# Performance work log

Measured on AMD Instinct MI355X. Metric: run time of the kernel, lower is better.

The kernel has to match this reference:

```python
import jax, jax.numpy as jnp
import numpy as np

D_MODEL = 1024
NHEAD = 16
HEAD_DIM = D_MODEL // NHEAD
D_FF = 4096
EPS = 1e-5


def _layernorm(x, g, b):
    mu = jnp.mean(x, axis=-1, keepdims=True)
    var = jnp.mean(jnp.square(x - mu), axis=-1, keepdims=True)
    return (x - mu) * jax.lax.rsqrt(var + EPS) * g + b


def setup_inputs() -> dict:
    key = jax.random.key(0)
    ks = jax.random.split(key, 8)

    def xavier(k, shape):
        fan_out, fan_in = shape
        lim = np.sqrt(6.0 / (fan_in + fan_out))
        return jax.random.uniform(k, shape, jnp.float32, -lim, lim)

    x = jax.random.normal(ks[0], (4, 2048, D_MODEL), jnp.float32)
    return {
        "x": x,
        "Wq": xavier(ks[1], (D_MODEL, D_MODEL)), "bq": jnp.zeros((D_MODEL,), jnp.float32),
        "Wk": xavier(ks[2], (D_MODEL, D_MODEL)), "bk": jnp.zeros((D_MODEL,), jnp.float32),
        "Wv": xavier(ks[3], (D_MODEL, D_MODEL)), "bv": jnp.zeros((D_MODEL,), jnp.float32),
        "Wo": xavier(ks[4], (D_MODEL, D_MODEL)), "bo": jnp.zeros((D_MODEL,), jnp.float32),
        "W1": xavier(ks[5], (D_FF, D_MODEL)), "b1": jnp.zeros((D_FF,), jnp.float32),
        "W2": xavier(ks[6], (D_MODEL, D_FF)), "b2": jnp.zeros((D_MODEL,), jnp.float32),
        "ln1_g": jnp.ones((D_MODEL,), jnp.float32), "ln1_b": jnp.zeros((D_MODEL,), jnp.float32),
        "ln2_g": jnp.ones((D_MODEL,), jnp.float32), "ln2_b": jnp.zeros((D_MODEL,), jnp.float32),
    }


def reference(x, Wq, bq, Wk, bk, Wv, bv, Wo, bo, W1, b1, W2, b2, ln1_g, ln1_b, ln2_g, ln2_b):
    B, T, D = x.shape
    H, Hd = NHEAD, HEAD_DIM

    # --- attention sublayer (pre-LN) ---
    residual = x
    xn = _layernorm(x, ln1_g, ln1_b)
    # torch Linear: y = x @ W.T + b
    q = (xn @ Wq.T + bq).reshape(B, T, H, Hd).transpose(0, 2, 1, 3)  # [B,H,T,Hd]
    k = (xn @ Wk.T + bk).reshape(B, T, H, Hd).transpose(0, 2, 1, 3)
    v = (xn @ Wv.T + bv).reshape(B, T, H, Hd).transpose(0, 2, 1, 3)

    scale = Hd ** -0.5
    scores = jnp.einsum('bhqd,bhkd->bhqk', q, k) * scale  # [B,H,T,T]
    attn = jax.nn.softmax(scores, axis=-1)
    out = jnp.einsum('bhqk,bhkd->bhqd', attn, v)           # [B,H,T,Hd]
    out = out.transpose(0, 2, 1, 3).reshape(B, T, D)
    out = out @ Wo.T + bo
    x = residual + out

    # --- FFN sublayer (pre-LN) ---
    residual = x
    xn = _layernorm(x, ln2_g, ln2_b)
    h = jax.nn.relu(xn @ W1.T + b1)
    h = h @ W2.T + b2
    return residual + h
```

## Files before the change

### kernel.cpp

```cpp
#include <hip/hip_runtime.h>
#include <hip/hip_bf16.h>

using bf16 = __hip_bfloat16;
typedef __attribute__((ext_vector_type(8))) short bf16x8;
typedef __attribute__((ext_vector_type(4))) float f32x4;

#define D_MODEL 1024
#define NHEAD 16
#define HEAD_DIM 64
#define D_FF 4096
#define SEQ 2048
#define NTOK 8192

__device__ __forceinline__ void gload16(const void* g, void* l) {
  __builtin_amdgcn_global_load_lds((const __attribute__((address_space(1))) void*)g,
                                   (__attribute__((address_space(3))) void*)l, 16, 0, 0);
}

__device__ __forceinline__ unsigned pkbf16(float lo, float hi) {
  unsigned r;
  asm("v_cvt_pk_bf16_f32 %0, %1, %2" : "=v"(r) : "v"(lo), "v"(hi));
  return r;
}

__device__ __forceinline__ float fexp2(float x) {
  float r;
  asm("v_exp_f32 %0, %1" : "=v"(r) : "v"(x));
  return r;
}

__device__ __forceinline__ float max3f(float a, float b, float c) {
  return fmaxf(fmaxf(a, b), c);
}

__global__ __launch_bounds__(256) void cvt_all(
    const float* __restrict__ W1, const float* __restrict__ W2,
    const float* __restrict__ Wq, const float* __restrict__ Wk,
    const float* __restrict__ Wv, const float* __restrict__ Wo,
    bf16* __restrict__ w1_b, bf16* __restrict__ w2_b,
    bf16* __restrict__ wqkv, bf16* __restrict__ wo_b) {
  const int bid = blockIdx.x;
  const float* src;
  bf16* dst;
  int lb;
  if (bid < 4096) { src = W1; dst = w1_b; lb = bid; }
  else if (bid < 8192) { src = W2; dst = w2_b; lb = bid - 4096; }
  else {
    const int j = (bid - 8192) >> 10;
    lb = (bid - 8192) & 1023;
    if (j == 0) { src = Wq; dst = wqkv; }
    else if (j == 1) { src = Wk; dst = wqkv + 1048576; }
    else if (j == 2) { src = Wv; dst = wqkv + 2097152; }
    else { src = Wo; dst = wo_b; }
  }
  const int i = (lb * 256 + threadIdx.x) * 4;
  const float4 v = *(const float4*)&src[i];
  dst[i + 0] = __float2bfloat16(v.x);
  dst[i + 1] = __float2bfloat16(v.y);
  dst[i + 2] = __float2bfloat16(v.z);
  dst[i + 3] = __float2bfloat16(v.w);
}

__global__ __launch_bounds__(256) void layernorm_kernel(
    const float* __restrict__ xin, const float* __restrict__ g,
    const float* __restrict__ bta, bf16* __restrict__ out) {
  const int row = blockIdx.x, t = threadIdx.x;
  const float4 v = *(const float4*)&xin[(size_t)row * D_MODEL + t * 4];
  float s = v.x + v.y + v.z + v.w;
#pragma unroll
  for (int m = 1; m < 64; m <<= 1) s += __shfl_xor(s, m);
  __shared__ float red[4], red2[4];
  const int w = t >> 6, l = t & 63;
  if (l == 0) red[w] = s;
  __syncthreads();
  const float mu = (red[0] + red[1] + red[2] + red[3]) * (1.f / 1024.f);
  const float d0 = v.x - mu, d1 = v.y - mu, d2 = v.z - mu, d3 = v.w - mu;
  float q = d0 * d0 + d1 * d1 + d2 * d2 + d3 * d3;
#pragma unroll
  for (int m = 1; m < 64; m <<= 1) q += __shfl_xor(q, m);
  if (l == 0) red2[w] = q;
  __syncthreads();
  const float var = (red2[0] + red2[1] + red2[2] + red2[3]) * (1.f / 1024.f);
  const float rs = rsqrtf(var + 1e-5f);
  const float4 gg = *(const float4*)&g[t * 4];
  const float4 bb = *(const float4*)&bta[t * 4];
  bf16* o = out + (size_t)row * D_MODEL + t * 4;
  o[0] = __float2bfloat16(d0 * rs * gg.x + bb.x);
  o[1] = __float2bfloat16(d1 * rs * gg.y + bb.y);
  o[2] = __float2bfloat16(d2 * rs * gg.z + bb.z);
  o[3] = __float2bfloat16(d3 * rs * gg.w + bb.w);
}

template <int MODE>
__global__ __launch_bounds__(512, 2) void gemmA(
    const bf16* __restrict__ A, const bf16* __restrict__ Bw,
    const float* __restrict__ bias0, const float* __restrict__ bias1,
    const float* __restrict__ bias2,
    void* __restrict__ out, int M, int N, int K) {
  constexpr int ASZ = 256 * 128;
  constexpr int TILE = ASZ + 256 * 128;
  __shared__ __align__(16) char smem[2 * TILE];

  const int t = threadIdx.x;
  const int l = t & 63, l15 = l & 15, l4 = (l >> 4) & 3;
  const int w = t >> 6, wm = w >> 2, wn = w & 3;
  const int gx = gridDim.x;
  const int nwg = gx * gridDim.y;
  const int bid0 = blockIdx.y * gx + blockIdx.x;
  const int bid = (bid0 & 7) * (nwg >> 3) + (bid0 >> 3);
  const int m0 = (bid / gx) * 256, n0 = (bid % gx) * 256;

  const int sr = t >> 3;
  const int scol = 8 * ((t & 7) ^ (sr & 7));
  const int swz = (l15 & 7) << 4;
  int coff[2];
  coff[0] = (l4 * 16) ^ swz;
  coff[1] = (64 + l4 * 16) ^ swz;

#define ST_A(j, kb, buf)                                          \
  gload16(&A[(size_t)(m0 + (j) * 64 + sr) * K + (kb) + scol],     \
          (void*)(smem + (buf) * TILE + (j) * 8192 + t * 16))
#define ST_B(j, kb, buf)                                          \
  gload16(&Bw[(size_t)(n0 + (j) * 64 + sr) * K + (kb) + scol],    \
          (void*)(smem + (buf) * TILE + ASZ + (j) * 8192 + t * 16))

  f32x4 acc[8][4] = {};
  const int NTm = K >> 6;

  ST_A(0, 0, 0); ST_A(2, 0, 0);
  ST_B(0, 0, 0); ST_B(1, 0, 0); ST_B(2, 0, 0); ST_B(3, 0, 0);
  ST_A(1, 0, 0); ST_A(3, 0, 0);
  asm volatile("s_waitcnt vmcnt(2)" ::: "memory");
  __builtin_amdgcn_s_barrier();

#define PHASE_A(p)                                                                 \
  {                                                                                \
    constexpr int kk = (p) & 1;                                                    \
    constexpr int mh = ((p) >> 1) * 4;                                             \
    bf16x8 af[4], bf[4];                                                           \
    _Pragma("unroll") for (int m = 0; m < 4; ++m)                                  \
      af[m] = *(const bf16x8*)(cb + (wm * 128 + (mh + m) * 16 + l15) * 128 +       \
                               coff[kk]);                                          \
    _Pragma("unroll") for (int n = 0; n < 4; ++n)                                  \
      bf[n] = *(const bf16x8*)(cb + ASZ + (wn * 64 + n * 16 + l15) * 128 +         \
                               coff[kk]);                                          \
    if (hasNext) {                                                                 \
      if ((p) == 0) { ST_A(0, kbn, nb); ST_A(2, kbn, nb); }                        \
      else if ((p) == 1) { ST_B(0, kbn, nb); ST_B(1, kbn, nb); }                   \
      else if ((p) == 2) { ST_B(2, kbn, nb); ST_B(3, kbn, nb); }                   \
      else { ST_A(1, kbn, nb); ST_A(3, kbn, nb); }                                 \
    }                                                                              \
    __builtin_amdgcn_s_barrier();                                                  \
    asm volatile("s_waitcnt lgkmcnt(0)" ::: "memory");                             \
    __builtin_amdgcn_sched_barrier(0);                                             \
    __builtin_amdgcn_s_setprio(1);                                                 \
    _Pragma("unroll") for (int m = 0; m < 4; ++m)                                  \
      _Pragma("unroll") for (int n = 0; n < 4; ++n)                                \
        acc[mh + m][n] = __builtin_amdgcn_mfma_f32_16x16x32_bf16(                  \
            af[m], bf[n], acc[mh + m][n], 0, 0, 0);                                \
    __builtin_amdgcn_s_setprio(0);                                                 \
    if ((p) == 1) {                                                                \
      if (hasNext) asm volatile("s_waitcnt vmcnt(4)" ::: "memory");                \
      else asm volatile("s_waitcnt vmcnt(0)" ::: "memory");                        \
    }                                                                              \
    if ((p) == 3 && hasNext)                                                       \
      asm volatile("s_waitcnt vmcnt(2)" ::: "memory");                             \
    __builtin_amdgcn_s_barrier();                                                  \
  }

  for (int kt = 0; kt < NTm; ++kt) {
    const char* cb = smem + (kt & 1) * TILE;
    const int nb = (kt & 1) ^ 1;
    const int kbn = (kt + 1) << 6;
    const bool hasNext = (kt + 1 < NTm);
    PHASE_A(0) PHASE_A(1) PHASE_A(2) PHASE_A(3)
  }
#undef PHASE_A
#undef ST_A
#undef ST_B

#pragma unroll
  for (int mf = 0; mf < 8; ++mf) {
#pragma unroll
    for (int nf = 0; nf < 4; ++nf) {
      const int col = n0 + wn * 64 + nf * 16 + l15;
      float bb;
      if constexpr (MODE == 0) {
        const int sel = col >> 10;
        const float* bp = (sel == 0) ? bias0 : ((sel == 1) ? bias1 : bias2);
        bb = bp[col & 1023];
      } else {
        bb = bias0[col];
      }
#pragma unroll
      for (int r = 0; r < 4; ++r) {
        const int row = m0 + wm * 128 + mf * 16 + l4 * 4 + r;
        float y = acc[mf][nf][r] + bb;
        if constexpr (MODE == 1) y = fmaxf(y, 0.f);
        if constexpr (MODE == 0) {
          const int sel = col >> 10;
          const int c10 = col & 1023;
          const size_t dst = (size_t)sel * (NTOK * 1024) +
                             (size_t)((row >> 11) * NHEAD + (c10 >> 6)) * (SEQ * HEAD_DIM) +
                             (size_t)(row & (SEQ - 1)) * HEAD_DIM + (c10 & 63);
          ((bf16*)out)[dst] = __float2bfloat16(y);
        } else {
          ((bf16*)out)[(size_t)row * N + col] = __float2bfloat16(y);
        }
      }
    }
  }
}

__global__ __launch_bounds__(512, 2) void gemmB(
    const bf16* __restrict__ A, const bf16* __restrict__ Bw,
    const float* __restrict__ bias, const float* __restrict__ res,
    float* __restrict__ out, int M, int N, int K) {
  constexpr int ASZ = 128 * 128;
  constexpr int TILE = ASZ + 256 * 128;
  __shared__ __align__(16) char smem[3 * TILE];

  const int t = threadIdx.x;
  const int l = t & 63, l15 = l & 15, l4 = (l >> 4) & 3;
  const int w = t >> 6, wm = w >> 2, wn = w & 3;
  const int gx = gridDim.x;
  const int nwg = gx * gridDim.y;
  const int bid0 = blockIdx.y * gx + blockIdx.x;
  const int bid = (bid0 & 7) * (nwg >> 3) + (bid0 >> 3);
  const int m0 = (bid / gx) * 128, n0 = (bid % gx) * 256;

  const int sr = t >> 3;
  const int scol = 8 * ((t & 7) ^ (sr & 7));
  const int swz = (l15 & 7) << 4;
  int coff[2];
  coff[0] = (l4 * 16) ^ swz;
  coff[1] = (64 + l4 * 16) ^ swz;

#define ST_A(j, kb, buf)                                          \
  gload16(&A[(size_t)(m0 + (j) * 64 + sr) * K + (kb) + scol],     \
          (void*)(smem + (buf) * TILE + (j) * 8192 + t * 16))
#define ST_B(j, kb, buf)                                          \
  gload16(&Bw[(size_t)(n0 + (j) * 64 + sr) * K + (kb) + scol],    \
          (void*)(smem + (buf) * TILE + ASZ + (j) * 8192 + t * 16))

  f32x4 acc[4][4] = {};
  const int NTm = K >> 6;

  ST_B(0, 0, 0); ST_B(1, 0, 0); ST_B(2, 0, 0);
  ST_B(3, 0, 0); ST_A(0, 0, 0); ST_A(1, 0, 0);
  ST_B(0, 64, 1); ST_B(1, 64, 1); ST_B(2, 64, 1);
  ST_B(3, 64, 1); ST_A(0, 64, 1); ST_A(1, 64, 1);
  asm volatile("s_waitcnt vmcnt(6)" ::: "memory");
  __builtin_amdgcn_s_barrier();

#define PHASE_B(p)                                                                 \
  {                                                                                \
    constexpr int kk = (p);                                                        \
    bf16x8 af[4], bf[4];                                                           \
    _Pragma("unroll") for (int m = 0; m < 4; ++m)                                  \
      af[m] = *(const bf16x8*)(cb + (wm * 64 + m * 16 + l15) * 128 + coff[kk]);    \
    _Pragma("unroll") for (int n = 0; n < 4; ++n)                                  \
      bf[n] = *(const bf16x8*)(cb + ASZ + (wn * 64 + n * 16 + l15) * 128 +         \
                               coff[kk]);                                          \
    if (iss) {                                                                     \
      if ((p) == 0) { ST_B(0, kbn, nb); ST_B(1, kbn, nb); ST_B(2, kbn, nb); }      \
      else { ST_B(3, kbn, nb); ST_A(0, kbn, nb); ST_A(1, kbn, nb); }               \
    }                                                                              \
    __builtin_amdgcn_s_barrier();                                                  \
    asm volatile("s_waitcnt lgkmcnt(0)" ::: "memory");                             \
    __builtin_amdgcn_sched_barrier(0);                                             \
    __builtin_amdgcn_s_setprio(1);                                                 \
    _Pragma("unroll") for (int m = 0; m < 4; ++m)                                  \
      _Pragma("unroll") for (int n = 0; n < 4; ++n)                                \
        acc[m][n] = __builtin_amdgcn_mfma_f32_16x16x32_bf16(                       \
            af[m], bf[n], acc[m][n], 0, 0, 0);                                     \
    __builtin_amdgcn_s_setprio(0);                                                 \
    if ((p) == 1) {                                                                \
      if (iss) asm volatile("s_waitcnt vmcnt(6)" ::: "memory");                    \
      else asm volatile("s_waitcnt vmcnt(0)" ::: "memory");                        \
    }                                                                              \
    __builtin_amdgcn_s_barrier();                                                  \
  }

  for (int kt = 0; kt < NTm; ++kt) {
    const char* cb = smem + (kt % 3) * TILE;
    const int nb = (kt + 2) % 3;
    const int kbn = (kt + 2) << 6;
    const bool iss = (kt + 2 < NTm);
    PHASE_B(0) PHASE_B(1)
  }
#undef PHASE_B
#undef ST_A
#undef ST_B

#pragma unroll
  for (int mf = 0; mf < 4; ++mf) {
#pragma unroll
    for (int nf = 0; nf < 4; ++nf) {
      const int col = n0 + wn * 64 + nf * 16 + l15;
      const float bb = bias[col];
#pragma unroll
      for (int r = 0; r < 4; ++r) {
        const int row = m0 + wm * 64 + mf * 16 + l4 * 4 + r;
        out[(size_t)row * N + col] = acc[mf][nf][r] + bb + res[(size_t)row * N + col];
      }
    }
  }
}

#define SCL 0.18033688011112042f
#define NT (SEQ / 64)

__global__ __launch_bounds__(256) void flash_attn(
    const bf16* __restrict__ Q, const bf16* __restrict__ K,
    const bf16* __restrict__ V, bf16* __restrict__ O) {
  __shared__ char smem[32768];
  const int t = threadIdx.x;
  const int w = t >> 6, l = t & 63;
  const int l15 = l & 15, l4 = l >> 4;
  const int bid0 = blockIdx.y * 16 + blockIdx.x;
  const int bid = (bid0 & 7) * 128 + (bid0 >> 3);
  const int bx = bid & 15, bh = bid >> 4;
  const size_t base = (size_t)bh * (SEQ * HEAD_DIM);
  const int q0 = bx * 128 + w * 32;
  const int dV = w * 16 + l15;

  int krow[4], kswz[4];
#pragma unroll
  for (int ni = 0; ni < 4; ++ni) {
    const int kr = (ni >> 1) * 32 + (ni & 1) * 4 + (l15 >> 2) * 8 + (l15 & 3);
    krow[ni] = kr * 128;
    kswz[ni] = ((kr & 3) | (((kr >> 3) & 1) << 2)) << 4;
  }

  bf16x8 qf[2][2];
#pragma unroll
  for (int mi = 0; mi < 2; ++mi)
#pragma unroll
    for (int kk = 0; kk < 2; ++kk)
      qf[mi][kk] = *(const bf16x8*)&Q[base + (size_t)(q0 + mi * 16 + l15) * 64 + kk * 32 + l4 * 8];

  bf16x8 ones;
#pragma unroll
  for (int j = 0; j < 8; ++j) ones[j] = (short)0x3F80;

  f32x4 accO[2][4] = {};
  float m_run[2], l_run[2];
#pragma unroll
  for (int mi = 0; mi < 2; ++mi) { m_run[mi] = -1e30f; l_run[mi] = 0.f; }

  short vg[16];

  const int r0 = t >> 3;
  const int c0 = 8 * ((t & 7) ^ ((r0 & 3) | (((r0 >> 3) & 1) << 2)));
  const int r1 = r0 + 32;
  const int c1 = 8 * ((t & 7) ^ ((r1 & 3) | (((r1 >> 3) & 1) << 2)));
  const short* kg0 = (const short*)K + base + r0 * 64 + c0;
  const short* kg1 = (const short*)K + base + r1 * 64 + c1;
  const short* vp0 = (const short*)V + base + (l4 * 8) * 64 + dV;
  const short* vp1 = vp0 + 2048;

#define STAGE_K(bufofs)                                          \
  {                                                              \
    gload16(kg0, (void*)(smem + (bufofs) + w * 1024));           \
    gload16(kg1, (void*)(smem + (bufofs) + 4096 + w * 1024));    \
    kg0 += 4096; kg1 += 4096;                                    \
  }

#define V_GATHER()                                               \
  {                                                              \
    _Pragma("unroll") for (int j_ = 0; j_ < 8; ++j_) {           \
      vg[j_] = vp0[j_ * 64];                                     \
      vg[8 + j_] = vp1[j_ * 64];                                 \
    }                                                            \
    vp0 += 4096; vp1 += 4096;                                    \
  }

#define VT_WRITE(bufofs)                                                          \
  {                                                                               \
    _Pragma("unroll") for (int h_ = 0; h_ < 2; ++h_) {                            \
      bf16x8 vv;                                                                  \
      _Pragma("unroll") for (int j_ = 0; j_ < 8; ++j_) vv[j_] = vg[h_ * 8 + j_];  \
      const int kb_ = (h_ * 64 + l4 * 16) ^ ((dV & 7) << 4);                      \
      *(bf16x8*)(smem + (bufofs) + dV * 128 + kb_) = vv;                          \
    }                                                                             \
  }

  STAGE_K(0);
  V_GATHER();
  VT_WRITE(16384);
  __syncthreads();

  for (int it = 0; it < NT; ++it) {
    const int cur = it & 1;
    const char* Kb = (const char*)smem + cur * 8192;
    const char* Vb = (const char*)smem + 16384 + cur * 8192;
    const bool pre = (it + 1 < NT);
    if (pre) {
      STAGE_K((cur ^ 1) * 8192);
      V_GATHER();
    }

    bf16x8 kf[2][4];
#pragma unroll
    for (int kk = 0; kk < 2; ++kk)
#pragma unroll
      for (int ni = 0; ni < 4; ++ni)
        kf[kk][ni] = *(const bf16x8*)(Kb + krow[ni] + ((kk * 64 + l4 * 16) ^ kswz[ni]));

    unsigned pw[2][8];
#pragma unroll
    for (int mi = 0; mi < 2; ++mi) {
      f32x4 s[4] = {};
      __builtin_amdgcn_s_setprio(1);
#pragma unroll
      for (int kk = 0; kk < 2; ++kk)
#pragma unroll
        for (int ni = 0; ni < 4; ++ni)
          s[ni] = __builtin_amdgcn_mfma_f32_16x16x32_bf16(kf[kk][ni], qf[mi][kk], s[ni], 0, 0, 0);
      __builtin_amdgcn_s_setprio(0);

      const float t0 = max3f(s[0][0], s[0][1], s[0][2]);
      const float t1 = max3f(s[0][3], s[1][0], s[1][1]);
      const float t2 = max3f(s[1][2], s[1][3], s[2][0]);
      const float t3 = max3f(s[2][1], s[2][2], s[2][3]);
      const float t4 = max3f(s[3][0], s[3][1], s[3][2]);
      float mx = fmaxf(max3f(t1, t2, t3), fmaxf(t4, fmaxf(t0, s[3][3])));
      mx = fmaxf(mx, __shfl_xor(mx, 16));
      mx = fmaxf(mx, __shfl_xor(mx, 32));
      const float mxs = mx * SCL;
      if (__any(mxs > m_run[mi] + 8.f)) {
        const float mn = fmaxf(m_run[mi], mxs);
        const float c = fexp2(m_run[mi] - mn);
        m_run[mi] = mn;
        l_run[mi] *= c;
#pragma unroll
        for (int ni = 0; ni < 4; ++ni)
#pragma unroll
          for (int r = 0; r < 4; ++r) accO[mi][ni][r] *= c;
      }
#pragma unroll
      for (int ni = 0; ni < 4; ++ni)
#pragma unroll
        for (int r = 0; r < 4; ++r)
          s[ni][r] = fexp2(fmaf(s[ni][r], SCL, -m_run[mi]));
#pragma unroll
      for (int kk = 0; kk < 2; ++kk)
#pragma unroll
        for (int jj = 0; jj < 4; ++jj) {
          const int ni = 2 * kk + (jj >> 1);
          pw[mi][kk * 4 + jj] = pkbf16(s[ni][2 * (jj & 1)], s[ni][2 * (jj & 1) + 1]);
        }
    }

    f32x4 zz[2] = {};
#pragma unroll
    for (int kk = 0; kk < 2; ++kk) {
      bf16x8 vf[4];
#pragma unroll
      for (int ni = 0; ni < 4; ++ni)
        vf[ni] = *(const bf16x8*)(Vb + (ni * 16 + l15) * 128 +
                                  ((kk * 64 + l4 * 16) ^ ((l15 & 7) << 4)));
#pragma unroll
      for (int mi = 0; mi < 2; ++mi) {
        union { unsigned u[4]; bf16x8 h; } pb;
#pragma unroll
        for (int jj = 0; jj < 4; ++jj) pb.u[jj] = pw[mi][kk * 4 + jj];
        __builtin_amdgcn_s_setprio(1);
#pragma unroll
        for (int ni = 0; ni < 4; ++ni)
          accO[mi][ni] = __builtin_amdgcn_mfma_f32_16x16x32_bf16(vf[ni], pb.h, accO[mi][ni], 0, 0, 0);
        zz[mi] = __builtin_amdgcn_mfma_f32_16x16x32_bf16(ones, pb.h, zz[mi], 0, 0, 0);
        __builtin_amdgcn_s_setprio(0);
      }
    }
#pragma unroll
    for (int mi = 0; mi < 2; ++mi) l_run[mi] += zz[mi][0];

    if (pre) VT_WRITE(16384 + (cur ^ 1) * 8192);
    __syncthreads();
  }

  char* ob = smem + w * 4096;
#pragma unroll
  for (int mi = 0; mi < 2; ++mi) {
    const float inv = 1.f / l_run[mi];
    const int qr = mi * 16 + l15;
    const int sw = (qr & 7) << 4;
#pragma unroll
    for (int ni = 0; ni < 4; ++ni)
#pragma unroll
      for (int rr = 0; rr < 2; ++rr) {
        const unsigned pk = pkbf16(accO[mi][ni][2 * rr] * inv, accO[mi][ni][2 * rr + 1] * inv);
        *(unsigned*)(ob + qr * 128 + ((ni * 32 + l4 * 8 + 4 * rr) ^ sw)) = pk;
      }
  }
  asm volatile("s_waitcnt lgkmcnt(0)" ::: "memory");
  __builtin_amdgcn_sched_barrier(0);

  const int b = bh >> 4, h = bh & 15;
  const int hr = l >> 1, hf = l & 1;
  const size_t orow = ((size_t)b * SEQ + bx * 128 + w * 32 + hr) * D_MODEL + h * HEAD_DIM + hf * 32;
#pragma unroll
  for (int c = 0; c < 4; ++c) {
    bf16x8 vv = *(const bf16x8*)(ob + hr * 128 + (((hf * 64) + c * 16) ^ ((hr & 7) << 4)));
    *(bf16x8*)&O[orow + c * 8] = vv;
  }
}

extern "C" void kernel_launch(void* const* d_in, const int* in_sizes, int n_in,
                              void* d_out, int out_size, void* d_ws, size_t ws_size,
                              hipStream_t stream) {
  const float* x     = (const float*)d_in[0];
  const float* Wq    = (const float*)d_in[1];
  const float* bq    = (const float*)d_in[2];
  const float* Wk    = (const float*)d_in[3];
  const float* bk    = (const float*)d_in[4];
  const float* Wv    = (const float*)d_in[5];
  const float* bv    = (const float*)d_in[6];
  const float* Wo    = (const float*)d_in[7];
  const float* bo    = (const float*)d_in[8];
  const float* W1    = (const float*)d_in[9];
  const float* b1    = (const float*)d_in[10];
  const float* W2    = (const float*)d_in[11];
  const float* b2    = (const float*)d_in[12];
  const float* ln1_g = (const float*)d_in[13];
  const float* ln1_b = (const float*)d_in[14];
  const float* ln2_g = (const float*)d_in[15];
  const float* ln2_b = (const float*)d_in[16];

  const size_t MB = 1ull << 20;
  char* ws = (char*)d_ws;
  bf16* wqkv = (bf16*)(ws + 0 * MB);
  bf16* wo_b = (bf16*)(ws + 6 * MB);
  bf16* w1_b = (bf16*)(ws + 8 * MB);
  bf16* w2_b = (bf16*)(ws + 16 * MB);
  bf16* xn   = (bf16*)(ws + 24 * MB);
  bf16* qb   = (bf16*)(ws + 40 * MB);
  bf16* kbuf = (bf16*)(ws + 56 * MB);
  bf16* vb   = (bf16*)(ws + 72 * MB);
  bf16* hb   = (bf16*)(ws + 40 * MB);
  float* x1  = (float*)(ws + 104 * MB);

  cvt_all<<<12288, 256, 0, stream>>>(W1, W2, Wq, Wk, Wv, Wo, w1_b, w2_b, wqkv, wo_b);

  layernorm_kernel<<<NTOK, 256, 0, stream>>>(x, ln1_g, ln1_b, xn);

  gemmA<0><<<dim3(3072 / 256, NTOK / 256), 512, 0, stream>>>(
      xn, wqkv, bq, bk, bv, qb, NTOK, 3072, 1024);

  flash_attn<<<dim3(SEQ / 128, 4 * NHEAD), 256, 0, stream>>>(qb, kbuf, vb, xn);

  gemmB<<<dim3(1024 / 256, NTOK / 128), 512, 0, stream>>>(
      xn, wo_b, bo, x, x1, NTOK, 1024, 1024);

  layernorm_kernel<<<NTOK, 256, 0, stream>>>(x1, ln2_g, ln2_b, xn);

  gemmA<1><<<dim3(D_FF / 256, NTOK / 256), 512, 0, stream>>>(
      xn, w1_b, b1, b1, b1, hb, NTOK, D_FF, 1024);

  gemmB<<<dim3(1024 / 256, NTOK / 128), 512, 0, stream>>>(
      hb, w2_b, b2, x1, (float*)d_out, NTOK, 1024, D_FF);
}
```

Before: 397.9 us.

## Double flash-attention query tile to 256 rows with 512-thread blocks

The attention kernel now runs 8 waves per block covering 256 query rows instead of 4 waves covering 128. Each K/V tile staged in shared memory is therefore reused by twice as many queries, which halves global K/V traffic per query. K staging and the V transpose-gather are redistributed so each thread loads one 16-byte K chunk and one 8-element V column slice. The grid halves to 512 blocks, which lowers the block count relative to CU count and may hurt latency hiding or tail balance.

```diff
diff --git a/kernel.cpp b/kernel.cpp
--- a/kernel.cpp
+++ b/kernel.cpp
@@ -311,19 +311,18 @@
 #define SCL 0.18033688011112042f
 #define NT (SEQ / 64)
 
-__global__ __launch_bounds__(256) void flash_attn(
+__global__ __launch_bounds__(512) void flash_attn(
     const bf16* __restrict__ Q, const bf16* __restrict__ K,
     const bf16* __restrict__ V, bf16* __restrict__ O) {
   __shared__ char smem[32768];
   const int t = threadIdx.x;
   const int w = t >> 6, l = t & 63;
   const int l15 = l & 15, l4 = l >> 4;
-  const int bid0 = blockIdx.y * 16 + blockIdx.x;
-  const int bid = (bid0 & 7) * 128 + (bid0 >> 3);
-  const int bx = bid & 15, bh = bid >> 4;
+  const int bid0 = blockIdx.y * 8 + blockIdx.x;
+  const int bid = (bid0 & 7) * 64 + (bid0 >> 3);
+  const int bx = bid & 7, bh = bid >> 3;
   const size_t base = (size_t)bh * (SEQ * HEAD_DIM);
-  const int q0 = bx * 128 + w * 32;
-  const int dV = w * 16 + l15;
+  const int q0 = bx * 256 + w * 32;
 
   int krow[4], kswz[4];
 #pragma unroll
@@ -349,41 +348,35 @@
 #pragma unroll
   for (int mi = 0; mi < 2; ++mi) { m_run[mi] = -1e30f; l_run[mi] = 0.f; }
 
-  short vg[16];
+  short vg[8];
 
   const int r0 = t >> 3;
   const int c0 = 8 * ((t & 7) ^ ((r0 & 3) | (((r0 >> 3) & 1) << 2)));
-  const int r1 = r0 + 32;
-  const int c1 = 8 * ((t & 7) ^ ((r1 & 3) | (((r1 >> 3) & 1) << 2)));
-  const short* kg0 = (const short*)K + base + r0 * 64 + c0;
-  const short* kg1 = (const short*)K + base + r1 * 64 + c1;
-  const short* vp0 = (const short*)V + base + (l4 * 8) * 64 + dV;
-  const short* vp1 = vp0 + 2048;
+  const short* kg = (const short*)K + base + r0 * 64 + c0;
+  const int dv = t & 63;
+  const int kb8 = (t >> 6) * 8;
+  const short* vp = (const short*)V + base + (size_t)kb8 * 64 + dv;
+  const int vtbyte = dv * 128 + ((kb8 * 2) ^ ((dv & 7) << 4));
 
 #define STAGE_K(bufofs)                                          \
   {                                                              \
-    gload16(kg0, (void*)(smem + (bufofs) + w * 1024));           \
-    gload16(kg1, (void*)(smem + (bufofs) + 4096 + w * 1024));    \
-    kg0 += 4096; kg1 += 4096;                                    \
+    gload16(kg, (void*)(smem + (bufofs) + w * 1024));            \
+    kg += 4096;                                                  \
   }
 
 #define V_GATHER()                                               \
   {                                                              \
-    _Pragma("unroll") for (int j_ = 0; j_ < 8; ++j_) {           \
-      vg[j_] = vp0[j_ * 64];                                     \
-      vg[8 + j_] = vp1[j_ * 64];                                 \
-    }                                                            \
-    vp0 += 4096; vp1 += 4096;                                    \
-  }
-
-#define VT_WRITE(bufofs)                                                          \
-  {                                                                               \
-    _Pragma("unroll") for (int h_ = 0; h_ < 2; ++h_) {                            \
-      bf16x8 vv;                                                                  \
-      _Pragma("unroll") for (int j_ = 0; j_ < 8; ++j_) vv[j_] = vg[h_ * 8 + j_];  \
-      const int kb_ = (h_ * 64 + l4 * 16) ^ ((dV & 7) << 4);                      \
-      *(bf16x8*)(smem + (bufofs) + dV * 128 + kb_) = vv;                          \
-    }                                                                             \
+    _Pragma("unroll") for (int j_ = 0; j_ < 8; ++j_)             \
+        vg[j_] = vp[j_ * 64];                                    \
+    vp += 4096;                                                  \
+  }
+
+#define VT_WRITE(bufofs)                                         \
+  {                                                              \
+    bf16x8 vv;                                                   \
+    _Pragma("unroll") for (int j_ = 0; j_ < 8; ++j_)             \
+        vv[j_] = vg[j_];                                         \
+    *(bf16x8*)(smem + (bufofs) + vtbyte) = vv;                   \
   }
 
   STAGE_K(0);
@@ -500,7 +493,7 @@
 
   const int b = bh >> 4, h = bh & 15;
   const int hr = l >> 1, hf = l & 1;
-  const size_t orow = ((size_t)b * SEQ + bx * 128 + w * 32 + hr) * D_MODEL + h * HEAD_DIM + hf * 32;
+  const size_t orow = ((size_t)b * SEQ + bx * 256 + w * 32 + hr) * D_MODEL + h * HEAD_DIM + hf * 32;
 #pragma unroll
   for (int c = 0; c < 4; ++c) {
     bf16x8 vv = *(const bf16x8*)(ob + hr * 128 + (((hf * 64) + c * 16) ^ ((hr & 7) << 4)));
@@ -549,7 +542,7 @@
   gemmA<0><<<dim3(3072 / 256, NTOK / 256), 512, 0, stream>>>(
       xn, wqkv, bq, bk, bv, qb, NTOK, 3072, 1024);
 
-  flash_attn<<<dim3(SEQ / 128, 4 * NHEAD), 256, 0, stream>>>(qb, kbuf, vb, xn);
+  flash_attn<<<dim3(SEQ / 256, 4 * NHEAD), 512, 0, stream>>>(qb, kbuf, vb, xn);
 
   gemmB<<<dim3(1024 / 256, NTOK / 128), 512, 0, stream>>>(
       xn, wo_b, bo, x, x1, NTOK, 1024, 1024);
```

Result: faster. 385.9 us (-3.0%).
